# Kernel tuning notes

Hardware: AMD Instinct MI355X
Metric: run time of the kernel (lower is better)

Reference implementation:

```python
import jax, jax.numpy as jnp
import numpy as np

N = 50000   # nodes
E = 800000  # edges (before self loops)
V = 30000   # vocab
D = 128     # emb_dim == hidden_dim
G = 64      # graphs in batch
L = 2       # num_layers
NEG_SLOPE = 0.2
LN_EPS = 1e-5


def setup_inputs() -> dict:
    key = jax.random.key(0)
    ks = jax.random.split(key, 12)
    node_ids = jax.random.randint(ks[0], (N,), 0, V)
    edge_index = jax.random.randint(ks[1], (2, E), 0, N)
    edge_weight = jax.random.uniform(ks[2], (E,), dtype=jnp.float32)
    batch = jnp.sort(jax.random.randint(ks[3], (N,), 0, G))
    s = 0.05
    emb = (jax.random.normal(ks[4], (V, D), dtype=jnp.float32) * s).at[0].set(0.0)  # padding_idx=0
    ln_g = jnp.ones((L, D), jnp.float32)
    ln_b = jnp.zeros((L, D), jnp.float32)
    att_w = jax.random.normal(ks[5], (L, 2 * D), dtype=jnp.float32) * s  # Linear(2D,1,bias=False)
    w1 = jax.random.normal(ks[6], (L, D, D), dtype=jnp.float32) * s
    b1 = jnp.zeros((L, D), jnp.float32)
    w2 = jax.random.normal(ks[7], (L, D, D), dtype=jnp.float32) * s
    b2 = jnp.zeros((L, D), jnp.float32)
    eps = jnp.zeros((L,), jnp.float32)  # trainable eps, init 0
    wh1 = jax.random.normal(ks[8], (D, D // 2), dtype=jnp.float32) * s
    bh1 = jnp.zeros((D // 2,), jnp.float32)
    wh2 = jax.random.normal(ks[9], (D // 2, 2), dtype=jnp.float32) * s
    bh2 = jnp.zeros((2,), jnp.float32)
    return dict(node_ids=node_ids, edge_index=edge_index, edge_weight=edge_weight, batch=batch,
                emb=emb, ln_g=ln_g, ln_b=ln_b, att_w=att_w, w1=w1, b1=b1, w2=w2, b2=b2,
                eps=eps, wh1=wh1, bh1=bh1, wh2=wh2, bh2=bh2)


def _layer_norm(x, g, b):
    mu = jnp.mean(x, axis=-1, keepdims=True)
    var = jnp.mean(jnp.square(x - mu), axis=-1, keepdims=True)
    return (x - mu) * jax.lax.rsqrt(var + LN_EPS) * g + b


def _conv(x, src, dst, ew, aw, W1, B1, W2, B2, e):
    # attention score: cat([x_i, x_j]) @ aw  ==  x_i @ aw[:D] + x_j @ aw[D:]
    score = x[dst] @ aw[:D] + x[src] @ aw[D:]            # [E2]
    score = jnp.where(score >= 0, score, NEG_SLOPE * score)  # leaky_relu(0.2)
    smax = jax.ops.segment_max(score, dst, num_segments=N)   # per-target max (all nodes have self loop)
    ex = jnp.exp(score - smax[dst])
    denom = jax.ops.segment_sum(ex, dst, num_segments=N)
    alpha = ex / (denom[dst] + 1e-16)                    # segment softmax (PyG softmax)
    alpha = alpha * ew                                   # edge weights (dropout is identity at eval)
    agg = jax.ops.segment_sum(alpha[:, None] * x[src], dst, num_segments=N)  # scatter-add messages
    out = (1.0 + e) * x + agg                            # GIN update
    return jax.nn.relu(out @ W1 + B1) @ W2 + B2          # conv MLP


def reference(node_ids, edge_index, edge_weight, batch, emb, ln_g, ln_b, att_w,
              w1, b1, w2, b2, eps, wh1, bh1, wh2, bh2):
    x = emb[node_ids]                                    # [N, D]
    loop = jnp.arange(N, dtype=edge_index.dtype)
    src = jnp.concatenate([edge_index[0], loop])         # add_self_loops
    dst = jnp.concatenate([edge_index[1], loop])
    ew = jnp.concatenate([edge_weight, jnp.ones((N,), edge_weight.dtype)])
    for l in range(L):
        x = _layer_norm(x, ln_g[l], ln_b[l])
        x = _conv(x, src, dst, ew, att_w[l], w1[l], b1[l], w2[l], b2[l], eps[l])
        x = jax.nn.relu(x)
    # global_mean_pool
    ones = jnp.ones((N,), x.dtype)
    counts = jax.ops.segment_sum(ones, batch, num_segments=G)
    g = jax.ops.segment_sum(x, batch, num_segments=G) / jnp.maximum(counts, 1.0)[:, None]
    # head MLP -> [G, 2]
    return jax.nn.relu(g @ wh1 + bh1) @ wh2 + bh2
```

## Files before the change

kernel.cpp:

```cpp
#include <hip/hip_runtime.h>

#define NN 50000
#define NPAD 50048
#define DD 128
#define GG 64
#define NBLK 49

typedef __attribute__((ext_vector_type(8))) short short8;
typedef __attribute__((ext_vector_type(8))) unsigned short ushort8;
typedef __attribute__((ext_vector_type(4))) float f32x4;

__device__ __forceinline__ unsigned short f2bf(float f){
  union { float f; unsigned u; } x; x.f = f;
  unsigned r = x.u + 0x7fffu + ((x.u >> 16) & 1u);
  return (unsigned short)(r >> 16);
}
__device__ __forceinline__ float bf2f(unsigned short h){
  union { unsigned u; float f; } x; x.u = ((unsigned)h) << 16;
  return x.f;
}
__device__ __forceinline__ unsigned short f2h(float f){
  union { _Float16 h; unsigned short u; } x; x.h = (_Float16)f; return x.u;
}
__device__ __forceinline__ float h2f(unsigned short u){
  union { _Float16 h; unsigned short u; } x; x.u = u; return (float)x.h;
}
__device__ __forceinline__ f32x4 mfma16(short8 a, short8 b, f32x4 c){
  return __builtin_amdgcn_mfma_f32_16x16x32_bf16(a, b, c, 0, 0, 0);
}

__device__ __forceinline__ float wave_reduce_sum(float v){
  #pragma unroll
  for (int off = 32; off; off >>= 1) v += __shfl_xor(v, off, 64);
  return v;
}
__device__ __forceinline__ float wave_reduce_max(float v){
  #pragma unroll
  for (int off = 32; off; off >>= 1) v = fmaxf(v, __shfl_xor(v, off, 64));
  return v;
}

__global__ __launch_bounds__(256) void gather_ln_kernel(const int* __restrict__ ids,
    const float* __restrict__ emb,
    const float* __restrict__ gamma, const float* __restrict__ beta,
    const float* __restrict__ aw,
    float* __restrict__ x, unsigned short* __restrict__ xhf,
    float* __restrict__ sd, float* __restrict__ ss, float* __restrict__ selfsc){
  int n = (blockIdx.x * 256 + threadIdx.x) >> 6;
  int lane = threadIdx.x & 63;
  if (n >= NN) return;
  int id = ids[n];
  float2 v = *(const float2*)&emb[(size_t)id * DD + lane * 2];
  float s  = wave_reduce_sum(v.x + v.y);
  float sq = wave_reduce_sum(v.x * v.x + v.y * v.y);
  float mu  = s * (1.0f / 128.0f);
  float var = sq * (1.0f / 128.0f) - mu * mu;
  float rs  = rsqrtf(var + 1e-5f);
  float2 g = *(const float2*)&gamma[lane * 2];
  float2 b = *(const float2*)&beta[lane * 2];
  float2 y;
  y.x = (v.x - mu) * rs * g.x + b.x;
  y.y = (v.y - mu) * rs * g.y + b.y;
  *(float2*)&x[(size_t)n * DD + lane * 2] = y;
  unsigned pk = (unsigned)f2h(y.x) | ((unsigned)f2h(y.y) << 16);
  ((unsigned*)xhf)[(size_t)n * 64 + lane] = pk;
  float2 a1 = *(const float2*)&aw[lane * 2];
  float2 a2 = *(const float2*)&aw[DD + lane * 2];
  float pd = wave_reduce_sum(y.x * a1.x + y.y * a1.y);
  float ps = wave_reduce_sum(y.x * a2.x + y.y * a2.y);
  if (lane == 0){
    sd[n] = pd; ss[n] = ps;
    float sc = pd + ps;
    selfsc[n] = sc >= 0.f ? sc : 0.2f * sc;
  }
}

__global__ __launch_bounds__(256) void pack_w_kernel(const float* __restrict__ w1,
    const float* __restrict__ w2, short* __restrict__ wph, short* __restrict__ wpl){
  int i = blockIdx.x * 256 + threadIdx.x;
  int m = i >> 14, k = (i >> 7) & 127, c = i & 127;
  const float* src = (m & 1) ? w2 : w1;
  float v = src[((size_t)(m >> 1) * 128 + k) * 128 + c];
  unsigned short h = f2bf(v);
  float lo = v - bf2f(h);
  int idx = (m << 14) + ((k >> 3) << 10) + (c << 3) + (k & 7);
  wph[idx] = (short)h;
  wpl[idx] = (short)f2bf(lo);
}

__global__ __launch_bounds__(256) void count_kernel(const int* __restrict__ dst,
    int* __restrict__ cnt, int E, int Q){
  int t = blockIdx.x * 256 + threadIdx.x;
  if (t >= Q) return;
  int e0 = t, e1 = t + Q, e2 = t + 2 * Q, e3 = t + 3 * Q;
  int d0 = (e0 < E) ? dst[e0] : -1;
  int d1 = (e1 < E) ? dst[e1] : -1;
  int d2 = (e2 < E) ? dst[e2] : -1;
  int d3 = (e3 < E) ? dst[e3] : -1;
  if (d0 >= 0) atomicAdd(&cnt[d0], 1);
  if (d1 >= 0) atomicAdd(&cnt[d1], 1);
  if (d2 >= 0) atomicAdd(&cnt[d2], 1);
  if (d3 >= 0) atomicAdd(&cnt[d3], 1);
}

__global__ __launch_bounds__(256) void scan1_kernel(const int* __restrict__ cnt,
    int* __restrict__ rp, int* __restrict__ bsum){
  __shared__ int wsum[4];
  int tid = threadIdx.x, lane = tid & 63, wid = tid >> 6;
  int base = blockIdx.x * 1024 + tid * 4;
  int4 v = {0,0,0,0};
  if (base < NN) v = *(const int4*)&cnt[base];
  int tsum = v.x + v.y + v.z + v.w;
  int incl = tsum;
  #pragma unroll
  for (int off = 1; off < 64; off <<= 1){
    int t = __shfl_up(incl, off, 64);
    if (lane >= off) incl += t;
  }
  if (lane == 63) wsum[wid] = incl;
  __syncthreads();
  int woff = 0;
  for (int w = 0; w < wid; ++w) woff += wsum[w];
  int excl = woff + incl - tsum;
  if (base < NN){
    int4 o;
    o.x = excl; o.y = excl + v.x; o.z = excl + v.x + v.y; o.w = excl + v.x + v.y + v.z;
    *(int4*)&rp[base] = o;
  }
  if (tid == 0) bsum[blockIdx.x] = wsum[0] + wsum[1] + wsum[2] + wsum[3];
}

__global__ __launch_bounds__(64) void scan2_kernel(int* __restrict__ bsum, int* __restrict__ rp){
  int lane = threadIdx.x;
  int v = (lane < NBLK) ? bsum[lane] : 0;
  int incl = v;
  #pragma unroll
  for (int off = 1; off < 64; off <<= 1){
    int t = __shfl_up(incl, off, 64);
    if (lane >= off) incl += t;
  }
  if (lane < NBLK) bsum[lane] = incl - v;
  if (lane == 63) rp[NN] = incl;
}

__global__ __launch_bounds__(256) void scan3_kernel(const int* __restrict__ bsum,
    int* __restrict__ rp, int* __restrict__ cursor){
  int base = blockIdx.x * 1024 + threadIdx.x * 4;
  if (base >= NN) return;
  int add = bsum[blockIdx.x];
  int4 t = *(const int4*)&rp[base];
  t.x += add; t.y += add; t.z += add; t.w += add;
  *(int4*)&rp[base] = t;
  *(int4*)&cursor[base] = t;
}

__global__ __launch_bounds__(256) void scatter_kernel(const int* __restrict__ src,
    const int* __restrict__ dst, const float* __restrict__ ew,
    int* __restrict__ cursor, unsigned* __restrict__ csr, int E, int Q){
  int t = blockIdx.x * 256 + threadIdx.x;
  if (t >= Q) return;
  int e0 = t, e1 = t + Q, e2 = t + 2 * Q, e3 = t + 3 * Q;
  int d0 = (e0 < E) ? dst[e0] : -1;
  int d1 = (e1 < E) ? dst[e1] : -1;
  int d2 = (e2 < E) ? dst[e2] : -1;
  int d3 = (e3 < E) ? dst[e3] : -1;
  unsigned r0 = 0, r1 = 0, r2 = 0, r3 = 0;
  if (d0 >= 0) r0 = (unsigned)src[e0] | ((unsigned)f2h(ew[e0]) << 16);
  if (d1 >= 0) r1 = (unsigned)src[e1] | ((unsigned)f2h(ew[e1]) << 16);
  if (d2 >= 0) r2 = (unsigned)src[e2] | ((unsigned)f2h(ew[e2]) << 16);
  if (d3 >= 0) r3 = (unsigned)src[e3] | ((unsigned)f2h(ew[e3]) << 16);
  int p0 = (d0 >= 0) ? atomicAdd(&cursor[d0], 1) : 0;
  int p1 = (d1 >= 0) ? atomicAdd(&cursor[d1], 1) : 0;
  int p2 = (d2 >= 0) ? atomicAdd(&cursor[d2], 1) : 0;
  int p3 = (d3 >= 0) ? atomicAdd(&cursor[d3], 1) : 0;
  if (d0 >= 0) csr[p0] = r0;
  if (d1 >= 0) csr[p1] = r1;
  if (d2 >= 0) csr[p2] = r2;
  if (d3 >= 0) csr[p3] = r3;
}

__global__ __launch_bounds__(256) void wgt_kernel(
    const int* __restrict__ row_ptr, const unsigned* __restrict__ csr,
    const float* __restrict__ sd, const float* __restrict__ ss,
    const float* __restrict__ selfsc,
    const float* __restrict__ eps_arr, int layer,
    float* __restrict__ csr_w, float* __restrict__ coef){
  int n = (blockIdx.x * 256 + threadIdx.x) >> 6;
  int lane = threadIdx.x & 63;
  if (n >= NN) return;
  int beg = row_ptr[n], end = row_ptr[n + 1];
  float sdn = sd[n];
  float sf = selfsc[n];
  float m = sf;
  for (int j = beg + lane; j < end; j += 64){
    unsigned e = csr[j];
    float sc = sdn + ss[e & 0xFFFFu];
    sc = sc >= 0.f ? sc : 0.2f * sc;
    m = fmaxf(m, sc);
  }
  m = wave_reduce_max(m);
  float dsum = 0.f;
  for (int j = beg + lane; j < end; j += 64){
    unsigned e = csr[j];
    float sc = sdn + ss[e & 0xFFFFu];
    sc = sc >= 0.f ? sc : 0.2f * sc;
    dsum += expf(sc - m);
  }
  dsum = wave_reduce_sum(dsum);
  float exself = expf(sf - m);
  dsum += exself;
  float inv = 1.0f / (dsum + 1e-16f);
  for (int j = beg + lane; j < end; j += 64){
    unsigned e = csr[j];
    float sc = sdn + ss[e & 0xFFFFu];
    sc = sc >= 0.f ? sc : 0.2f * sc;
    csr_w[j] = expf(sc - m) * inv * h2f((unsigned short)(e >> 16));
  }
  if (lane == 0) coef[n] = 1.0f + eps_arr[layer] + exself * inv;
}

__global__ __launch_bounds__(256) void agg2_kernel(const float* __restrict__ x,
    const unsigned short* __restrict__ xhf,
    const int* __restrict__ row_ptr, const unsigned* __restrict__ csr,
    const float* __restrict__ csr_w,
    const float* __restrict__ coef, short* __restrict__ aggH, short* __restrict__ aggL){
  int n = (blockIdx.x * 256 + threadIdx.x) >> 6;
  int lane = threadIdx.x & 63;
  if (n >= NN) return;
  int grp = lane >> 4, sub = lane & 15;
  int beg = row_ptr[n], end = row_ptr[n + 1];
  float a[8] = {0,0,0,0,0,0,0,0};
  int j = beg + grp;
  for (; j + 4 < end; j += 8){
    int   s0 = csr[j] & 0xFFFFu;     float w0 = csr_w[j];
    int   s1 = csr[j + 4] & 0xFFFFu; float w1 = csr_w[j + 4];
    ushort8 u0 = *(const ushort8*)&xhf[(size_t)s0 * DD + sub * 8];
    ushort8 u1 = *(const ushort8*)&xhf[(size_t)s1 * DD + sub * 8];
    #pragma unroll
    for (int i = 0; i < 8; ++i) a[i] = fmaf(w0, h2f(u0[i]), a[i]);
    #pragma unroll
    for (int i = 0; i < 8; ++i) a[i] = fmaf(w1, h2f(u1[i]), a[i]);
  }
  if (j < end){
    int s0 = csr[j] & 0xFFFFu; float w0 = csr_w[j];
    ushort8 u0 = *(const ushort8*)&xhf[(size_t)s0 * DD + sub * 8];
    #pragma unroll
    for (int i = 0; i < 8; ++i) a[i] = fmaf(w0, h2f(u0[i]), a[i]);
  }
  #pragma unroll
  for (int mask = 16; mask <= 32; mask <<= 1){
    #pragma unroll
    for (int i = 0; i < 8; ++i) a[i] += __shfl_xor(a[i], mask, 64);
  }
  if (grp == 0){
    float c = coef[n];
    const float4* xr = (const float4*)&x[(size_t)n * DD + sub * 8];
    float4 x0 = xr[0], x1 = xr[1];
    a[0] = fmaf(c, x0.x, a[0]); a[1] = fmaf(c, x0.y, a[1]);
    a[2] = fmaf(c, x0.z, a[2]); a[3] = fmaf(c, x0.w, a[3]);
    a[4] = fmaf(c, x1.x, a[4]); a[5] = fmaf(c, x1.y, a[5]);
    a[6] = fmaf(c, x1.z, a[6]); a[7] = fmaf(c, x1.w, a[7]);
    short8 H, L;
    #pragma unroll
    for (int i = 0; i < 8; ++i){
      unsigned short h = f2bf(a[i]);
      H[i] = (short)h;
      L[i] = (short)f2bf(a[i] - bf2f(h));
    }
    *(short8*)&aggH[(size_t)n * DD + sub * 8] = H;
    *(short8*)&aggL[(size_t)n * DD + sub * 8] = L;
  }
}

template<int MODE>
__global__ __launch_bounds__(256) void mlp_mfma_kernel(
    const short* __restrict__ aH, const short* __restrict__ aL,
    const short* __restrict__ w1h, const short* __restrict__ w1l,
    const short* __restrict__ w2h, const short* __restrict__ w2l,
    const float* __restrict__ B1, const float* __restrict__ B2,
    const float* __restrict__ g2, const float* __restrict__ be2,
    const float* __restrict__ aw2,
    float* __restrict__ xout, unsigned short* __restrict__ xhf,
    float* __restrict__ sd, float* __restrict__ ss,
    float* __restrict__ selfsc){
  __shared__ __align__(16) short hh[64 * DD];
  __shared__ __align__(16) short hl[64 * DD];
  int tid = threadIdx.x;
  int w = tid >> 6, l = tid & 63;
  int g = l >> 4, c16 = l & 15;
  int base = blockIdx.x * 64;
  int rowA = base + w * 16 + c16;

  short8 a1h[4], a1l[4];
  #pragma unroll
  for (int ks = 0; ks < 4; ++ks){
    size_t off = (size_t)rowA * DD + ks * 32 + g * 8;
    a1h[ks] = *(const short8*)(aH + off);
    a1l[ks] = *(const short8*)(aL + off);
  }

  f32x4 acc[8];
  #pragma unroll
  for (int ct = 0; ct < 8; ++ct){
    f32x4 a = {0.f, 0.f, 0.f, 0.f};
    #pragma unroll
    for (int ks = 0; ks < 4; ++ks){
      int bo = (((ks * 4 + g) * 128) + ct * 16 + c16) * 8;
      short8 bh = *(const short8*)(w1h + bo);
      short8 bl = *(const short8*)(w1l + bo);
      a = mfma16(a1h[ks], bh, a);
      a = mfma16(a1l[ks], bh, a);
      a = mfma16(a1h[ks], bl, a);
    }
    acc[ct] = a;
  }

  #pragma unroll
  for (int ct = 0; ct < 8; ++ct){
    int col = ct * 16 + c16;
    float b = B1[col];
    #pragma unroll
    for (int r = 0; r < 4; ++r){
      int rl = w * 16 + g * 4 + r;
      float v = acc[ct][r] + b;
      v = v > 0.f ? v : 0.f;
      unsigned short h = f2bf(v);
      int idx = rl * DD + ((((col >> 3) ^ (rl & 7))) << 3) + (col & 7);
      hh[idx] = (short)h;
      hl[idx] = (short)f2bf(v - bf2f(h));
    }
  }
  __syncthreads();

  int rowL = w * 16 + c16;
  short8 a2h[4], a2l[4];
  #pragma unroll
  for (int ks = 0; ks < 4; ++ks){
    int chunk = ks * 4 + g;
    int idx = rowL * DD + ((chunk ^ (rowL & 7)) << 3);
    a2h[ks] = *(const short8*)&hh[idx];
    a2l[ks] = *(const short8*)&hl[idx];
  }

  #pragma unroll
  for (int ct = 0; ct < 8; ++ct){
    f32x4 a = {0.f, 0.f, 0.f, 0.f};
    #pragma unroll
    for (int ks = 0; ks < 4; ++ks){
      int bo = (((ks * 4 + g) * 128) + ct * 16 + c16) * 8;
      short8 bh = *(const short8*)(w2h + bo);
      short8 bl = *(const short8*)(w2l + bo);
      a = mfma16(a2h[ks], bh, a);
      a = mfma16(a2l[ks], bh, a);
      a = mfma16(a2h[ks], bl, a);
    }
    acc[ct] = a;
  }

  #pragma unroll
  for (int ct = 0; ct < 8; ++ct){
    int col = ct * 16 + c16;
    float b = B2[col];
    #pragma unroll
    for (int r = 0; r < 4; ++r){
      float v = acc[ct][r] + b;
      acc[ct][r] = v > 0.f ? v : 0.f;
    }
  }

  if (MODE == 1){
    #pragma unroll
    for (int ct = 0; ct < 8; ++ct){
      int col = ct * 16 + c16;
      #pragma unroll
      for (int r = 0; r < 4; ++r){
        int row = base + w * 16 + g * 4 + r;
        if (row < NN) xout[(size_t)row * DD + col] = acc[ct][r];
      }
    }
  } else {
    float s[4] = {0,0,0,0}, sq[4] = {0,0,0,0};
    #pragma unroll
    for (int ct = 0; ct < 8; ++ct)
      #pragma unroll
      for (int r = 0; r < 4; ++r){ float v = acc[ct][r]; s[r] += v; sq[r] += v * v; }
    #pragma unroll
    for (int off = 1; off < 16; off <<= 1){
      #pragma unroll
      for (int r = 0; r < 4; ++r){
        s[r]  += __shfl_xor(s[r],  off, 64);
        sq[r] += __shfl_xor(sq[r], off, 64);
      }
    }
    float mu[4], rs[4];
    #pragma unroll
    for (int r = 0; r < 4; ++r){
      mu[r] = s[r] * (1.f / 128.f);
      float var = sq[r] * (1.f / 128.f) - mu[r] * mu[r];
      rs[r] = rsqrtf(var + 1e-5f);
    }
    float pd[4] = {0,0,0,0}, ps[4] = {0,0,0,0};
    #pragma unroll
    for (int ct = 0; ct < 8; ++ct){
      int col = ct * 16 + c16;
      float gam = g2[col], bet = be2[col];
      float aa = aw2[col], ab = aw2[DD + col];
      #pragma unroll
      for (int r = 0; r < 4; ++r){
        float y = (acc[ct][r] - mu[r]) * rs[r] * gam + bet;
        acc[ct][r] = y;
        pd[r] += y * aa; ps[r] += y * ab;
      }
    }
    #pragma unroll
    for (int off = 1; off < 16; off <<= 1){
      #pragma unroll
      for (int r = 0; r < 4; ++r){
        pd[r] += __shfl_xor(pd[r], off, 64);
        ps[r] += __shfl_xor(ps[r], off, 64);
      }
    }
    #pragma unroll
    for (int ct = 0; ct < 8; ++ct){
      int col = ct * 16 + c16;
      #pragma unroll
      for (int r = 0; r < 4; ++r){
        int row = base + w * 16 + g * 4 + r;
        if (row < NN){
          float y = acc[ct][r];
          xout[(size_t)row * DD + col] = y;
          xhf[(size_t)row * DD + col] = f2h(y);
        }
      }
    }
    if (c16 == 0){
      #pragma unroll
      for (int r = 0; r < 4; ++r){
        int row = base + w * 16 + g * 4 + r;
        if (row < NN){
          sd[row] = pd[r]; ss[row] = ps[r];
          float sc = pd[r] + ps[r];
          selfsc[row] = sc >= 0.f ? sc : 0.2f * sc;
        }
      }
    }
  }
}

__global__ __launch_bounds__(128) void pool_kernel(const float* __restrict__ x,
    const int* __restrict__ batch, float* __restrict__ gsum, int* __restrict__ gcnt){
  int g = blockIdx.x >> 4, part = blockIdx.x & 15;
  int lo = 0, hi = NN;
  while (lo < hi){ int mid = (lo + hi) >> 1; if (batch[mid] < g) lo = mid + 1; else hi = mid; }
  int beg = lo;
  lo = beg; hi = NN;
  while (lo < hi){ int mid = (lo + hi) >> 1; if (batch[mid] < g + 1) lo = mid + 1; else hi = mid; }
  int end = lo;
  int cg = end - beg;
  int rb = beg + (int)((long long)cg * part / 16);
  int re = beg + (int)((long long)cg * (part + 1) / 16);
  int d = threadIdx.x;
  float s0 = 0.f, s1 = 0.f, s2 = 0.f, s3 = 0.f;
  int r = rb;
  for (; r + 3 < re; r += 4){
    s0 += x[(size_t)r * DD + d];
    s1 += x[(size_t)(r + 1) * DD + d];
    s2 += x[(size_t)(r + 2) * DD + d];
    s3 += x[(size_t)(r + 3) * DD + d];
  }
  for (; r < re; ++r) s0 += x[(size_t)r * DD + d];
  float sum = (s0 + s1) + (s2 + s3);
  atomicAdd(&gsum[g * DD + d], sum);
  if (d == 0 && part == 0) gcnt[g] = cg;
}

__global__ __launch_bounds__(256) void head_kernel(const float* __restrict__ gsum,
    const int* __restrict__ gcnt,
    const float* __restrict__ wh1, const float* __restrict__ bh1,
    const float* __restrict__ wh2, const float* __restrict__ bh2,
    float* __restrict__ outp){
  __shared__ float gm[GG * DD];
  __shared__ float h[GG * 64];
  int tid = threadIdx.x;
  for (int i = tid; i < GG * DD; i += 256){
    int g = i >> 7;
    int c = gcnt[g];
    gm[i] = gsum[i] / (float)(c > 0 ? c : 1);
  }
  __syncthreads();
  for (int i = tid; i < GG * 64; i += 256){
    int r = i >> 6, c = i & 63;
    float a0 = 0.f, a1 = 0.f;
    for (int k = 0; k < DD; k += 2){
      a0 = fmaf(gm[r * DD + k],     wh1[k * 64 + c],       a0);
      a1 = fmaf(gm[r * DD + k + 1], wh1[(k + 1) * 64 + c], a1);
    }
    float v = a0 + a1 + bh1[c];
    h[i] = v > 0.f ? v : 0.f;
  }
  __syncthreads();
  if (tid < GG * 2){
    int r = tid >> 1, c = tid & 1;
    float a = 0.f;
    for (int k = 0; k < 64; ++k) a = fmaf(h[r * 64 + k], wh2[k * 2 + c], a);
    outp[tid] = a + bh2[c];
  }
}

extern "C" void kernel_launch(void* const* d_in, const int* in_sizes, int n_in,
                              void* d_out, int out_size, void* d_ws, size_t ws_size,
                              hipStream_t stream){
  const int*   node_ids    = (const int*)  d_in[0];
  const int*   edge_index  = (const int*)  d_in[1];
  const float* edge_weight = (const float*)d_in[2];
  const int*   batch       = (const int*)  d_in[3];
  const float* emb         = (const float*)d_in[4];
  const float* ln_g        = (const float*)d_in[5];
  const float* ln_b        = (const float*)d_in[6];
  const float* att_w       = (const float*)d_in[7];
  const float* w1          = (const float*)d_in[8];
  const float* b1          = (const float*)d_in[9];
  const float* w2          = (const float*)d_in[10];
  const float* b2          = (const float*)d_in[11];
  const float* eps         = (const float*)d_in[12];
  const float* wh1         = (const float*)d_in[13];
  const float* bh1         = (const float*)d_in[14];
  const float* wh2         = (const float*)d_in[15];
  const float* bh2         = (const float*)d_in[16];
  int E = in_sizes[1] / 2;
  const int* srcp = edge_index;
  const int* dstp = edge_index + E;
  int Q = (E + 3) / 4;

  char* w = (char*)d_ws;
  float* x       = (float*)w; w += (size_t)NN * DD * 4;
  unsigned short* xhf = (unsigned short*)w; w += (size_t)NN * DD * 2;
  short* aggH    = (short*)w; w += (size_t)NPAD * DD * 2;
  short* aggL    = (short*)w; w += (size_t)NPAD * DD * 2;
  short* wph     = (short*)w; w += (size_t)4 * 16384 * 2;
  short* wpl     = (short*)w; w += (size_t)4 * 16384 * 2;
  float* sd      = (float*)w; w += (size_t)NN * 4;
  float* ssb     = (float*)w; w += (size_t)NN * 4;
  float* selfsc  = (float*)w; w += (size_t)NN * 4;
  float* coef    = (float*)w; w += (size_t)NN * 4;
  int*   cnt     = (int*)  w; w += (size_t)NN * 4;
  int*   row_ptr = (int*)  w; w += (size_t)(NN + 8) * 4;
  int*   cursor  = (int*)  w; w += (size_t)NN * 4;
  int*   bsum    = (int*)  w; w += (size_t)64 * 4;
  unsigned* csr  = (unsigned*)w; w += (size_t)E * 4;
  float* csr_w   = (float*)w; w += (size_t)E * 4;
  float* gsum    = (float*)w; w += (size_t)GG * DD * 4;
  int*   gcnt    = (int*)  w; w += (size_t)GG * 4;

  hipMemsetAsync(cnt, 0, (size_t)NN * 4, stream);
  hipMemsetAsync(gsum, 0, (size_t)GG * DD * 4, stream);

  count_kernel<<<(Q + 255) / 256, 256, 0, stream>>>(dstp, cnt, E, Q);
  scan1_kernel<<<NBLK, 256, 0, stream>>>(cnt, row_ptr, bsum);
  scan2_kernel<<<1, 64, 0, stream>>>(bsum, row_ptr);
  scan3_kernel<<<NBLK, 256, 0, stream>>>(bsum, row_ptr, cursor);
  scatter_kernel<<<(Q + 255) / 256, 256, 0, stream>>>(srcp, dstp, edge_weight, cursor, csr, E, Q);
  pack_w_kernel<<<256, 256, 0, stream>>>(w1, w2, wph, wpl);
  gather_ln_kernel<<<(NN + 3) / 4, 256, 0, stream>>>(node_ids, emb, ln_g, ln_b, att_w,
                                                     x, xhf, sd, ssb, selfsc);

  int mlp_grid = (NN + 63) / 64;
  wgt_kernel <<<(NN + 3) / 4, 256, 0, stream>>>(row_ptr, csr, sd, ssb, selfsc, eps, 0, csr_w, coef);
  agg2_kernel<<<(NN + 3) / 4, 256, 0, stream>>>(x, xhf, row_ptr, csr, csr_w, coef, aggH, aggL);
  mlp_mfma_kernel<0><<<mlp_grid, 256, 0, stream>>>(aggH, aggL,
      wph, wpl, wph + 16384, wpl + 16384, b1, b2,
      ln_g + DD, ln_b + DD, att_w + 2 * DD, x, xhf, sd, ssb, selfsc);
  wgt_kernel <<<(NN + 3) / 4, 256, 0, stream>>>(row_ptr, csr, sd, ssb, selfsc, eps, 1, csr_w, coef);
  agg2_kernel<<<(NN + 3) / 4, 256, 0, stream>>>(x, xhf, row_ptr, csr, csr_w, coef, aggH, aggL);
  mlp_mfma_kernel<1><<<mlp_grid, 256, 0, stream>>>(aggH, aggL,
      wph + 2 * 16384, wpl + 2 * 16384, wph + 3 * 16384, wpl + 3 * 16384,
      b1 + DD, b2 + DD, ln_g + DD, ln_b + DD, att_w + 2 * DD, x, xhf, sd, ssb, selfsc);

  pool_kernel<<<GG * 16, 128, 0, stream>>>(x, batch, gsum, gcnt);
  head_kernel<<<1, 256, 0, stream>>>(gsum, gcnt, wh1, bh1, wh2, bh2, (float*)d_out);
}
```

Baseline: 418.1 us.

## Split MLP tile across waves by output columns with 16-row blocks

The MLP kernel now gives each block 16 rows instead of 64, and its four waves split the 128 output columns (two 16-column tiles each) rather than each wave owning 16 rows. This multiplies the grid size and shrinks shared memory per block, raising parallelism and occupancy across CUs. The cost is cross-wave LayerNorm and attention-dot reductions through shared memory with extra barriers, and every block rereads the full weight set. Row bounds checks are removed because 50000 divides evenly by 16.

```diff
diff --git a/kernel.cpp b/kernel.cpp
--- a/kernel.cpp
+++ b/kernel.cpp
@@ -283,13 +283,15 @@
     float* __restrict__ xout, unsigned short* __restrict__ xhf,
     float* __restrict__ sd, float* __restrict__ ss,
     float* __restrict__ selfsc){
-  __shared__ __align__(16) short hh[64 * DD];
-  __shared__ __align__(16) short hl[64 * DD];
+  __shared__ __align__(16) short hh[16 * DD];
+  __shared__ __align__(16) short hl[16 * DD];
+  __shared__ float red0[4][16];
+  __shared__ float red1[4][16];
   int tid = threadIdx.x;
   int w = tid >> 6, l = tid & 63;
   int g = l >> 4, c16 = l & 15;
-  int base = blockIdx.x * 64;
-  int rowA = base + w * 16 + c16;
+  int base = blockIdx.x * 16;
+  int rowA = base + c16;
 
   short8 a1h[4], a1l[4];
   #pragma unroll
@@ -299,9 +301,10 @@
     a1l[ks] = *(const short8*)(aL + off);
   }
 
-  f32x4 acc[8];
-  #pragma unroll
-  for (int ct = 0; ct < 8; ++ct){
+  f32x4 acc[2];
+  #pragma unroll
+  for (int cti = 0; cti < 2; ++cti){
+    int ct = w * 2 + cti;
     f32x4 a = {0.f, 0.f, 0.f, 0.f};
     #pragma unroll
     for (int ks = 0; ks < 4; ++ks){
@@ -312,17 +315,17 @@
       a = mfma16(a1l[ks], bh, a);
       a = mfma16(a1h[ks], bl, a);
     }
-    acc[ct] = a;
-  }
-
-  #pragma unroll
-  for (int ct = 0; ct < 8; ++ct){
-    int col = ct * 16 + c16;
+    acc[cti] = a;
+  }
+
+  #pragma unroll
+  for (int cti = 0; cti < 2; ++cti){
+    int col = (w * 2 + cti) * 16 + c16;
     float b = B1[col];
     #pragma unroll
     for (int r = 0; r < 4; ++r){
-      int rl = w * 16 + g * 4 + r;
-      float v = acc[ct][r] + b;
+      int rl = g * 4 + r;
+      float v = acc[cti][r] + b;
       v = v > 0.f ? v : 0.f;
       unsigned short h = f2bf(v);
       int idx = rl * DD + ((((col >> 3) ^ (rl & 7))) << 3) + (col & 7);
@@ -332,7 +335,7 @@
   }
   __syncthreads();
 
-  int rowL = w * 16 + c16;
+  int rowL = c16;
   short8 a2h[4], a2l[4];
   #pragma unroll
   for (int ks = 0; ks < 4; ++ks){
@@ -343,7 +346,8 @@
   }
 
   #pragma unroll
-  for (int ct = 0; ct < 8; ++ct){
+  for (int cti = 0; cti < 2; ++cti){
+    int ct = w * 2 + cti;
     f32x4 a = {0.f, 0.f, 0.f, 0.f};
     #pragma unroll
     for (int ks = 0; ks < 4; ++ks){
@@ -354,94 +358,113 @@
       a = mfma16(a2l[ks], bh, a);
       a = mfma16(a2h[ks], bl, a);
     }
-    acc[ct] = a;
-  }
-
-  #pragma unroll
-  for (int ct = 0; ct < 8; ++ct){
-    int col = ct * 16 + c16;
+    acc[cti] = a;
+  }
+
+  #pragma unroll
+  for (int cti = 0; cti < 2; ++cti){
+    int col = (w * 2 + cti) * 16 + c16;
     float b = B2[col];
     #pragma unroll
     for (int r = 0; r < 4; ++r){
-      float v = acc[ct][r] + b;
-      acc[ct][r] = v > 0.f ? v : 0.f;
+      float v = acc[cti][r] + b;
+      acc[cti][r] = v > 0.f ? v : 0.f;
     }
   }
 
   if (MODE == 1){
     #pragma unroll
-    for (int ct = 0; ct < 8; ++ct){
-      int col = ct * 16 + c16;
-      #pragma unroll
-      for (int r = 0; r < 4; ++r){
-        int row = base + w * 16 + g * 4 + r;
-        if (row < NN) xout[(size_t)row * DD + col] = acc[ct][r];
+    for (int cti = 0; cti < 2; ++cti){
+      int col = (w * 2 + cti) * 16 + c16;
+      #pragma unroll
+      for (int r = 0; r < 4; ++r){
+        int row = base + g * 4 + r;
+        xout[(size_t)row * DD + col] = acc[cti][r];
       }
     }
   } else {
-    float s[4] = {0,0,0,0}, sq[4] = {0,0,0,0};
-    #pragma unroll
-    for (int ct = 0; ct < 8; ++ct)
-      #pragma unroll
-      for (int r = 0; r < 4; ++r){ float v = acc[ct][r]; s[r] += v; sq[r] += v * v; }
+    float s_p[4] = {0,0,0,0}, q_p[4] = {0,0,0,0};
+    #pragma unroll
+    for (int cti = 0; cti < 2; ++cti)
+      #pragma unroll
+      for (int r = 0; r < 4; ++r){ float v = acc[cti][r]; s_p[r] += v; q_p[r] += v * v; }
     #pragma unroll
     for (int off = 1; off < 16; off <<= 1){
       #pragma unroll
       for (int r = 0; r < 4; ++r){
-        s[r]  += __shfl_xor(s[r],  off, 64);
-        sq[r] += __shfl_xor(sq[r], off, 64);
-      }
-    }
+        s_p[r] += __shfl_xor(s_p[r], off, 64);
+        q_p[r] += __shfl_xor(q_p[r], off, 64);
+      }
+    }
+    if (c16 == 0){
+      #pragma unroll
+      for (int r = 0; r < 4; ++r){
+        red0[w][g * 4 + r] = s_p[r];
+        red1[w][g * 4 + r] = q_p[r];
+      }
+    }
+    __syncthreads();
     float mu[4], rs[4];
     #pragma unroll
     for (int r = 0; r < 4; ++r){
-      mu[r] = s[r] * (1.f / 128.f);
-      float var = sq[r] * (1.f / 128.f) - mu[r] * mu[r];
+      int rt = g * 4 + r;
+      float S = (red0[0][rt] + red0[1][rt]) + (red0[2][rt] + red0[3][rt]);
+      float Q = (red1[0][rt] + red1[1][rt]) + (red1[2][rt] + red1[3][rt]);
+      mu[r] = S * (1.f / 128.f);
+      float var = Q * (1.f / 128.f) - mu[r] * mu[r];
       rs[r] = rsqrtf(var + 1e-5f);
     }
-    float pd[4] = {0,0,0,0}, ps[4] = {0,0,0,0};
-    #pragma unroll
-    for (int ct = 0; ct < 8; ++ct){
-      int col = ct * 16 + c16;
+    __syncthreads();
+    float pd_p[4] = {0,0,0,0}, ps_p[4] = {0,0,0,0};
+    #pragma unroll
+    for (int cti = 0; cti < 2; ++cti){
+      int col = (w * 2 + cti) * 16 + c16;
       float gam = g2[col], bet = be2[col];
       float aa = aw2[col], ab = aw2[DD + col];
       #pragma unroll
       for (int r = 0; r < 4; ++r){
-        float y = (acc[ct][r] - mu[r]) * rs[r] * gam + bet;
-        acc[ct][r] = y;
-        pd[r] += y * aa; ps[r] += y * ab;
+        float y = (acc[cti][r] - mu[r]) * rs[r] * gam + bet;
+        acc[cti][r] = y;
+        pd_p[r] += y * aa; ps_p[r] += y * ab;
       }
     }
     #pragma unroll
     for (int off = 1; off < 16; off <<= 1){
       #pragma unroll
       for (int r = 0; r < 4; ++r){
-        pd[r] += __shfl_xor(pd[r], off, 64);
-        ps[r] += __shfl_xor(ps[r], off, 64);
-      }
-    }
-    #pragma unroll
-    for (int ct = 0; ct < 8; ++ct){
-      int col = ct * 16 + c16;
-      #pragma unroll
-      for (int r = 0; r < 4; ++r){
-        int row = base + w * 16 + g * 4 + r;
-        if (row < NN){
-          float y = acc[ct][r];
-          xout[(size_t)row * DD + col] = y;
-          xhf[(size_t)row * DD + col] = f2h(y);
-        }
+        pd_p[r] += __shfl_xor(pd_p[r], off, 64);
+        ps_p[r] += __shfl_xor(ps_p[r], off, 64);
       }
     }
     if (c16 == 0){
       #pragma unroll
       for (int r = 0; r < 4; ++r){
-        int row = base + w * 16 + g * 4 + r;
-        if (row < NN){
-          sd[row] = pd[r]; ss[row] = ps[r];
-          float sc = pd[r] + ps[r];
-          selfsc[row] = sc >= 0.f ? sc : 0.2f * sc;
-        }
+        red0[w][g * 4 + r] = pd_p[r];
+        red1[w][g * 4 + r] = ps_p[r];
+      }
+    }
+    __syncthreads();
+    #pragma unroll
+    for (int cti = 0; cti < 2; ++cti){
+      int col = (w * 2 + cti) * 16 + c16;
+      #pragma unroll
+      for (int r = 0; r < 4; ++r){
+        int row = base + g * 4 + r;
+        float y = acc[cti][r];
+        xout[(size_t)row * DD + col] = y;
+        xhf[(size_t)row * DD + col] = f2h(y);
+      }
+    }
+    if (w == 0 && c16 == 0){
+      #pragma unroll
+      for (int r = 0; r < 4; ++r){
+        int rt = g * 4 + r;
+        int row = base + rt;
+        float pd = (red0[0][rt] + red0[1][rt]) + (red0[2][rt] + red0[3][rt]);
+        float ps = (red1[0][rt] + red1[1][rt]) + (red1[2][rt] + red1[3][rt]);
+        sd[row] = pd; ss[row] = ps;
+        float sc = pd + ps;
+        selfsc[row] = sc >= 0.f ? sc : 0.2f * sc;
       }
     }
   }
@@ -564,7 +587,7 @@
   gather_ln_kernel<<<(NN + 3) / 4, 256, 0, stream>>>(node_ids, emb, ln_g, ln_b, att_w,
                                                      x, xhf, sd, ssb, selfsc);
 
-  int mlp_grid = (NN + 63) / 64;
+  int mlp_grid = (NN + 15) / 16;
   wgt_kernel <<<(NN + 3) / 4, 256, 0, stream>>>(row_ptr, csr, sd, ssb, selfsc, eps, 0, csr_w, coef);
   agg2_kernel<<<(NN + 3) / 4, 256, 0, stream>>>(x, xhf, row_ptr, csr, csr_w, coef, aggH, aggL);
   mlp_mfma_kernel<0><<<mlp_grid, 256, 0, stream>>>(aggH, aggL,
```

New measurement: 412.9 us. About the same (-1.2%).
